# Optimization experiments

Measured on AMD Instinct MI355X. Metric: run time of the kernel, lower is better.

The kernel has to match this reference:

```python
import jax, jax.numpy as jnp
import numpy as np

S, B, T, D = 256, 32, 24, 512


def setup_inputs() -> dict:
    key = jax.random.key(0)
    ks = jax.random.split(key, 30)
    def lin(k, out_d, in_d):
        kw, kb = jax.random.split(k)
        w = jax.random.normal(kw, (out_d, in_d), jnp.float32) * 0.02
        b = jax.random.normal(kb, (out_d,), jnp.float32) * 0.02
        return w, b
    inp = {
        'context_output': jax.random.normal(ks[0], (S, B, D), jnp.float32),
        'context_hidden_state': jax.random.normal(ks[1], (B, D), jnp.float32),
        'question_output': jax.random.normal(ks[2], (T, B, D), jnp.float32),
        'question_hidden_state': jax.random.normal(ks[3], (B, D), jnp.float32),
        'image_output': jax.random.normal(ks[4], (S, B, D), jnp.float32),
        'image_hidden_state': jax.random.normal(ks[5], (B, D), jnp.float32),
    }
    inp['fc1_w'], inp['fc1_b'] = lin(ks[6], D, D)
    inp['fc2_w'], inp['fc2_b'] = lin(ks[7], D, D)
    inp['dm_w'], inp['dm_b'] = lin(ks[8], D, D)
    inp['ms_w'], inp['ms_b'] = lin(ks[9], 1, D)
    inp['rm_w'], inp['rm_b'] = lin(ks[10], D, D)
    inp['qm_w'], inp['qm_b'] = lin(ks[11], D, D)
    inp['rr_w'], inp['rr_b'] = lin(ks[12], D, D)
    inp['rg_w'], inp['rg_b'] = lin(ks[13], D, D)
    inp['qg_w'], inp['qg_b'] = lin(ks[14], D, D)
    return inp


def reference(context_output, context_hidden_state, question_output,
              question_hidden_state, image_output, image_hidden_state,
              fc1_w, fc1_b, fc2_w, fc2_b, dm_w, dm_b, ms_w, ms_b,
              rm_w, rm_b, qm_w, qm_b, rr_w, rr_b, rg_w, rg_b, qg_w, qg_b):
    # context_output/image_output: [S,B,D] -> co: [B,S,D]
    co = (jnp.einsum('sbd,ed->bse', context_output, fc1_w) + fc1_b
          + jnp.einsum('sbd,ed->bse', image_output, fc2_w) + fc2_b)
    # linear_dm(co) is loop-invariant; compute once (same math as original)
    co_dm = jnp.einsum('bsd,ed->bse', co, dm_w) + dm_b  # [B,S,D]

    def step(r, q):
        # r: [B,D] (the original's [B,1,D] memory), q: [B,D]
        add = (r @ rm_w.T + rm_b) + (q @ qm_w.T + qm_b)  # [B,D]
        m = jnp.tanh(co_dm + add[:, None, :])             # [B,S,D]
        logits = m @ ms_w.T + ms_b                        # [B,S,1]
        s = jax.nn.softmax(logits, axis=1)                # softmax over S
        r_new = jnp.sum(s * co, axis=1) + jnp.tanh(r @ rr_w.T + rr_b)
        return r_new, None

    r0 = jnp.zeros((B, D), co.dtype)
    r, _ = jax.lax.scan(step, r0, question_output)  # scan over T steps
    g = (r @ rg_w.T + rg_b) + (question_hidden_state @ qg_w.T + qg_b)
    return g
```

## Files before the change

### kernel.cpp

```cpp
#include <hip/hip_runtime.h>

#define S_DIM 256
#define B_DIM 32
#define T_DIM 24
#define D_DIM 512

typedef short short8 __attribute__((ext_vector_type(8)));
typedef unsigned short ushort8 __attribute__((ext_vector_type(8)));
typedef unsigned short ushort4v __attribute__((ext_vector_type(4)));
typedef float float4v __attribute__((ext_vector_type(4)));
typedef unsigned long long u64;

#define ATOM_ST64(p, v) __hip_atomic_store((p), (v), __ATOMIC_RELAXED, __HIP_MEMORY_SCOPE_AGENT)
#define ATOM_LD64(p)    __hip_atomic_load((p), __ATOMIC_RELAXED, __HIP_MEMORY_SCOPE_AGENT)

__device__ __forceinline__ float bf2f(unsigned short u) {
  union { unsigned int i; float f; } v; v.i = ((unsigned int)u) << 16; return v.f;
}
__device__ __forceinline__ unsigned short f2bf(float f) {
  union { float f; unsigned int i; } v; v.f = f;
  unsigned int i = v.i;
  return (unsigned short)((i + 0x7fffu + ((i >> 16) & 1u)) >> 16);
}
__device__ __forceinline__ float tanh_fast(float x) {
  float p = __builtin_amdgcn_exp2f(x * 2.885390082f);
  return 1.f - 2.f * __builtin_amdgcn_rcpf(1.f + p);
}
__device__ __forceinline__ void gload_lds16(const void* g, void* l) {
  __builtin_amdgcn_global_load_lds(
      (const __attribute__((address_space(1))) void*)g,
      (__attribute__((address_space(3))) void*)l, 16, 0, 0);
}
__device__ __forceinline__ u64 pack_tag(unsigned tag, float v) {
  union { float f; unsigned u; } c; c.f = v;
  return ((u64)tag << 32) | (u64)c.u;
}
__device__ __forceinline__ float unpack_val(u64 v) {
  union { unsigned u; float f; } c; c.u = (unsigned)v; return c.f;
}
__device__ __forceinline__ float poll_val(const u64* p, unsigned tag) {
  u64 v = ATOM_LD64(p);
  while ((unsigned)(v >> 32) != tag) { __builtin_amdgcn_s_sleep(1); v = ATOM_LD64(p); }
  return unpack_val(v);
}

__global__ __launch_bounds__(256)
void cvt_kernel(const float* __restrict__ s0, const float* __restrict__ s1,
                const float* __restrict__ s2, const float* __restrict__ s3,
                const float* __restrict__ s4,
                unsigned short* __restrict__ d0, unsigned short* __restrict__ d1,
                unsigned short* __restrict__ d2, unsigned short* __restrict__ d3,
                unsigned short* __restrict__ d4)
{
  const int idx = blockIdx.x * 256 + threadIdx.x;
  const float* s; unsigned short* d; int off;
  if (idx < 2097152) {
    off = idx & 1048575;
    if (idx < 1048576) { s = s0; d = d0; } else { s = s1; d = d1; }
  } else {
    const int k = (idx - 2097152) >> 16;
    off = (idx - 2097152) & 65535;
    if (k == 0)      { s = s2; d = d2; }
    else if (k == 1) { s = s3; d = d3; }
    else             { s = s4; d = d4; }
  }
  const float4v v = ((const float4v*)s)[off];
  ushort4v u;
  u[0] = f2bf(v[0]); u[1] = f2bf(v[1]); u[2] = f2bf(v[2]); u[3] = f2bf(v[3]);
  ((ushort4v*)d)[off] = u;
}

template<bool DUAL, bool PERMUTE>
__global__ __launch_bounds__(256)
void gemm_nt(const unsigned short* __restrict__ A1,
             const unsigned short* __restrict__ A2,
             const unsigned short* __restrict__ W1,
             const unsigned short* __restrict__ W2,
             const float* __restrict__ bias1,
             const float* __restrict__ bias2,
             unsigned short* __restrict__ out)
{
  __shared__ unsigned short At[128 * 32] __attribute__((aligned(16)));
  __shared__ unsigned short Bt[64 * 32] __attribute__((aligned(16)));

  const int tid  = threadIdx.x;
  const int wid  = tid >> 6;
  const int lane = tid & 63;
  const int bid = blockIdx.x;
  const int bm = ((bid & 7) << 3) | ((bid >> 3) & 7);
  const int bn = bid >> 6;
  const int wm = (wid & 1) * 64, wn = (wid >> 1) * 32;

  float4v acc[4][2];
#pragma unroll
  for (int i = 0; i < 4; ++i)
#pragma unroll
    for (int jj = 0; jj < 2; ++jj) acc[i][jj] = (float4v){0.f, 0.f, 0.f, 0.f};

  const int NK = DUAL ? 32 : 16;
  for (int it = 0; it < NK; ++it) {
    const int kk = it * 32;
    const unsigned short* As = A1;
    const unsigned short* Ws = W1;
    int ks = kk;
    if (DUAL && kk >= 512) { As = A2; Ws = W2; ks = kk - 512; }

    __syncthreads();
#pragma unroll
    for (int i = 0; i < 2; ++i)
      gload_lds16(As + (size_t)(bm * 128 + wid * 32 + i * 16 + (lane >> 2)) * 512 + ks + (lane & 3) * 8,
                  &At[(wid * 32 + i * 16) * 32]);
    gload_lds16(Ws + (size_t)(bn * 64 + wid * 16 + (lane >> 2)) * 512 + ks + (lane & 3) * 8,
                &Bt[(wid * 16) * 32]);
    __syncthreads();

    short8 fa[4], fb[2];
#pragma unroll
    for (int mi = 0; mi < 4; ++mi)
      fa[mi] = *(const short8*)&At[(wm + mi * 16 + (lane & 15)) * 32 + (lane >> 4) * 8];
#pragma unroll
    for (int ni = 0; ni < 2; ++ni)
      fb[ni] = *(const short8*)&Bt[(wn + ni * 16 + (lane & 15)) * 32 + (lane >> 4) * 8];
#pragma unroll
    for (int mi = 0; mi < 4; ++mi)
#pragma unroll
      for (int ni = 0; ni < 2; ++ni)
        acc[mi][ni] = __builtin_amdgcn_mfma_f32_16x16x32_bf16(fa[mi], fb[ni], acc[mi][ni], 0, 0, 0);
  }

#pragma unroll
  for (int mi = 0; mi < 4; ++mi) {
    const int row0 = wm + mi * 16 + (lane >> 4) * 4;
#pragma unroll
    for (int ni = 0; ni < 2; ++ni) {
      const int col = bn * 64 + wn + ni * 16 + (lane & 15);
      float bsum = 0.f;
      if (bias1) bsum += bias1[col];
      if (bias2) bsum += bias2[col];
#pragma unroll
      for (int i = 0; i < 4; ++i) {
        const int m = bm * 128 + row0 + i;
        const int orow = PERMUTE ? ((m & 31) * 256 + (m >> 5)) : m;
        out[(size_t)orow * 512 + col] = f2bf(acc[mi][ni][i] + bsum);
      }
    }
  }
}

__global__ __launch_bounds__(512)
void scan_kernel(const unsigned short* __restrict__ co,
                 const unsigned short* __restrict__ codm,
                 const float* __restrict__ qo,
                 u64* __restrict__ addT,
                 u64* __restrict__ rrtT,
                 u64* __restrict__ denT,
                 u64* __restrict__ pvecT,
                 const float* __restrict__ ms_w,
                 const float* __restrict__ rm_w,
                 const float* __restrict__ rr_w,
                 const float* __restrict__ rr_b,
                 const float* __restrict__ qm_w,
                 const float* __restrict__ qm_b,
                 const float* __restrict__ rm_b,
                 const float* __restrict__ qhs,
                 const float* __restrict__ rg_w,
                 const float* __restrict__ qg_w,
                 const float* __restrict__ rg_b,
                 const float* __restrict__ qg_b,
                 float* __restrict__ outg)
{
  __shared__ unsigned short scrS[32 * 520] __attribute__((aligned(16)));
  __shared__ float rS[512];
  __shared__ float addS[512] __attribute__((aligned(16)));
  __shared__ float msS[512] __attribute__((aligned(16)));
  __shared__ float partS[512];
  __shared__ float partR[512];
  __shared__ float rrtS[512];
  __shared__ float pvS[512];
  __shared__ float wS[32];
  __shared__ float rrbS[64];
  __shared__ float qmrmS[64];
  __shared__ float denS[8];
  __shared__ float qaddS[T_DIM * 64];

  const int tid  = threadIdx.x;
  const int wid  = tid >> 6;
  const int lane = tid & 63;
  const int b = blockIdx.x >> 3;
  const int j = blockIdx.x & 7;

  ushort8 rmp[8], rrp[8], qmp[8];
  for (int pass = 0; pass < 6; ++pass) {
    const float* Wsrc = (pass < 2) ? rm_w : (pass < 4) ? rr_w : qm_w;
    const int rbase = (pass & 1) * 32;
    for (int r = wid; r < 32; r += 8) {
      const float* src = &Wsrc[(size_t)(j * 64 + rbase + r) * 512 + lane * 8];
      float4v a = *(const float4v*)src;
      float4v c = *(const float4v*)(src + 4);
      ushort8 u8;
#pragma unroll
      for (int i = 0; i < 4; ++i) { u8[i] = f2bf(a[i]); u8[i + 4] = f2bf(c[i]); }
      *(ushort8*)&scrS[r * 520 + lane * 8] = u8;
    }
    __syncthreads();
    if ((lane >> 5) == (pass & 1)) {
      const int rloc = lane & 31;
#pragma unroll
      for (int u = 0; u < 8; ++u) {
        ushort8 v = *(const ushort8*)&scrS[rloc * 520 + wid * 64 + u * 8];
        if (pass < 2) rmp[u] = v; else if (pass < 4) rrp[u] = v; else qmp[u] = v;
      }
    }
    __syncthreads();
  }

  msS[tid] = ms_w[tid];
  if (tid < 64) {
    rrbS[tid]  = rr_b[j * 64 + tid];
    qmrmS[tid] = qm_b[j * 64 + tid] + rm_b[j * 64 + tid];
  }

  float* qoS = (float*)scrS;
  for (int half = 0; half < 2; ++half) {
    __syncthreads();
#pragma unroll
    for (int i = 0; i < 3; ++i) {
      const int f4 = tid + i * 512;
      const int tl = f4 >> 7, c4 = f4 & 127;
      ((float4v*)qoS)[f4] =
          *(const float4v*)&qo[((size_t)(half * 12 + tl) * 32 + b) * 512 + c4 * 4];
    }
    __syncthreads();
    for (int tl = 0; tl < 12; ++tl) {
      float p = 0.f;
#pragma unroll
      for (int u = 0; u < 8; ++u) {
        ushort8 w8 = qmp[u];
#pragma unroll
        for (int i2 = 0; i2 < 8; ++i2)
          p = fmaf(qoS[tl * 512 + wid * 64 + u * 8 + i2], bf2f(w8[i2]), p);
      }
      float* pbuf = (tl & 1) ? partR : partS;
      pbuf[wid * 64 + lane] = p;
      __syncthreads();
      if (wid == (tl & 1)) {
        float s = 0.f;
#pragma unroll
        for (int w2 = 0; w2 < 8; ++w2) s += pbuf[w2 * 64 + lane];
        qaddS[(half * 12 + tl) * 64 + lane] = s + qmrmS[lane];
      }
    }
    __syncthreads();
  }

  const size_t gbase = ((size_t)b * 256 + j * 32) * 512;
  for (int idx = tid; idx < 2048; idx += 512)
    *(ushort8*)&scrS[idx * 8] = *(const ushort8*)&codm[gbase + (size_t)idx * 8];
  const unsigned short* cdS = scrS;

  partS[tid] = 0.f;
  partR[tid] = 0.f;

  for (int t = 0; t < T_DIM; ++t) {
    const unsigned tagA = 2u * (unsigned)t + 1u;
    const unsigned tagB = 2u * (unsigned)t + 2u;
    __syncthreads();

    if (wid == 0) {
      float s = 0.f;
#pragma unroll
      for (int w2 = 0; w2 < 8; ++w2) s += partS[w2 * 64 + lane];
      s += qaddS[t * 64 + lane];
      ATOM_ST64(&addT[b * 512 + j * 64 + lane], pack_tag(tagA, s));
    } else if (wid == 1) {
      float s = 0.f;
#pragma unroll
      for (int w2 = 0; w2 < 8; ++w2) s += partR[w2 * 64 + lane];
      ATOM_ST64(&rrtT[(size_t)(t & 1) * (B_DIM * 512) + b * 512 + j * 64 + lane],
                pack_tag(tagA, tanh_fast(s + rrbS[lane])));
    }
    addS[tid] = poll_val(&addT[b * 512 + tid], tagA);
    __syncthreads();

#pragma unroll
    for (int q = 0; q < 4; ++q) {
      const int sl = wid * 4 + q;
      ushort8 cd8 = *(const ushort8*)&cdS[sl * 512 + lane * 8];
      float4v a0 = *(const float4v*)&addS[lane * 8];
      float4v a1 = *(const float4v*)&addS[lane * 8 + 4];
      float4v m0 = *(const float4v*)&msS[lane * 8];
      float4v m1 = *(const float4v*)&msS[lane * 8 + 4];
      float acc = 0.f;
#pragma unroll
      for (int i = 0; i < 4; ++i) {
        acc = fmaf(tanh_fast(bf2f(cd8[i]) + a0[i]), m0[i], acc);
        acc = fmaf(tanh_fast(bf2f(cd8[i + 4]) + a1[i]), m1[i], acc);
      }
#pragma unroll
      for (int off = 32; off > 0; off >>= 1) acc += __shfl_xor(acc, off, 64);
      if (lane == 0) wS[sl] = __builtin_amdgcn_exp2f(acc * 1.44269504f);
    }
    __syncthreads();

    {
      float accv = 0.f;
#pragma unroll 8
      for (int sl = 0; sl < 32; ++sl)
        accv = fmaf(wS[sl], bf2f(co[gbase + (size_t)sl * 512 + tid]), accv);
      ATOM_ST64(&pvecT[((size_t)b * 8 + j) * 512 + tid], pack_tag(tagB, accv));
    }
    float dv = 0.f;
    if (wid == 0) {
      dv = (lane < 32) ? wS[lane] : 0.f;
#pragma unroll
      for (int off = 32; off > 0; off >>= 1) dv += __shfl_xor(dv, off, 64);
    }
    __syncthreads();
    if (tid == 0) ATOM_ST64(&denT[b * 8 + j], pack_tag(tagB, dv));

    u64 rv64 = ATOM_LD64(&rrtT[(size_t)(t & 1) * (B_DIM * 512) + b * 512 + tid]);
    while ((unsigned)(rv64 >> 32) != tagA) {
      __builtin_amdgcn_s_sleep(1);
      rv64 = ATOM_LD64(&rrtT[(size_t)(t & 1) * (B_DIM * 512) + b * 512 + tid]);
    }
    rrtS[tid] = unpack_val(rv64);
    if (wid == 0 && lane < 8) denS[lane] = poll_val(&denT[b * 8 + lane], tagB);
    __syncthreads();

    u64 pv[8];
#pragma unroll
    for (int jj = 0; jj < 8; ++jj)
      pv[jj] = ATOM_LD64(&pvecT[((size_t)b * 8 + jj) * 512 + tid]);
    float am = 0.f, ar = 0.f;
#pragma unroll
    for (int u = 0; u < 8; ++u) {
      ushort8 wm8 = rmp[u], wr8 = rrp[u];
#pragma unroll
      for (int i2 = 0; i2 < 8; ++i2) {
        const float rv = rrtS[wid * 64 + u * 8 + i2];
        am = fmaf(rv, bf2f(wm8[i2]), am);
        ar = fmaf(rv, bf2f(wr8[i2]), ar);
      }
    }
    float sum = 0.f;
#pragma unroll
    for (int jj = 0; jj < 8; ++jj) {
      while ((unsigned)(pv[jj] >> 32) != tagB) {
        __builtin_amdgcn_s_sleep(1);
        pv[jj] = ATOM_LD64(&pvecT[((size_t)b * 8 + jj) * 512 + tid]);
      }
      sum += unpack_val(pv[jj]);
    }
    const float den = denS[0] + denS[1] + denS[2] + denS[3] +
                      denS[4] + denS[5] + denS[6] + denS[7];
    const float pvs = sum * __builtin_amdgcn_rcpf(den);
    pvS[tid] = pvs;
    rS[tid]  = pvs + rrtS[tid];
    __syncthreads();

#pragma unroll
    for (int u = 0; u < 8; ++u) {
      ushort8 wm8 = rmp[u], wr8 = rrp[u];
#pragma unroll
      for (int i2 = 0; i2 < 8; ++i2) {
        const float pvv = pvS[wid * 64 + u * 8 + i2];
        am = fmaf(pvv, bf2f(wm8[i2]), am);
        ar = fmaf(pvv, bf2f(wr8[i2]), ar);
      }
    }
    partS[wid * 64 + lane] = am;
    partR[wid * 64 + lane] = ar;
  }

  __syncthreads();
  addS[tid] = qhs[b * 512 + tid];
  __syncthreads();
  {
    const int e = j * 64 + lane;
    const float* rgp = rg_w + (size_t)e * 512 + wid * 64;
    const float* qgp = qg_w + (size_t)e * 512 + wid * 64;
    float acc = 0.f;
#pragma unroll
    for (int u = 0; u < 8; ++u) {
      float4v g0 = *(const float4v*)&rgp[u * 8];
      float4v g1 = *(const float4v*)&rgp[u * 8 + 4];
      float4v q0 = *(const float4v*)&qgp[u * 8];
      float4v q1 = *(const float4v*)&qgp[u * 8 + 4];
#pragma unroll
      for (int i2 = 0; i2 < 4; ++i2) {
        acc = fmaf(rS[wid * 64 + u * 8 + i2],     g0[i2], acc);
        acc = fmaf(rS[wid * 64 + u * 8 + 4 + i2], g1[i2], acc);
        acc = fmaf(addS[wid * 64 + u * 8 + i2],     q0[i2], acc);
        acc = fmaf(addS[wid * 64 + u * 8 + 4 + i2], q1[i2], acc);
      }
    }
    partS[wid * 64 + lane] = acc;
  }
  __syncthreads();
  if (wid == 0) {
    float s = 0.f;
#pragma unroll
    for (int w2 = 0; w2 < 8; ++w2) s += partS[w2 * 64 + lane];
    const int e = j * 64 + lane;
    s += rg_b[e] + qg_b[e];
    outg[b * 512 + e] = s;
  }
}

extern "C" void kernel_launch(void* const* d_in, const int* in_sizes, int n_in,
                              void* d_out, int out_size, void* d_ws, size_t ws_size,
                              hipStream_t stream)
{
  (void)in_sizes; (void)n_in; (void)out_size; (void)ws_size;
  const float* ctx  = (const float*)d_in[0];
  const float* qo   = (const float*)d_in[2];
  const float* qhs  = (const float*)d_in[3];
  const float* img  = (const float*)d_in[4];
  const float* fc1w = (const float*)d_in[6];
  const float* fc1b = (const float*)d_in[7];
  const float* fc2w = (const float*)d_in[8];
  const float* fc2b = (const float*)d_in[9];
  const float* dmw  = (const float*)d_in[10];
  const float* dmb  = (const float*)d_in[11];
  const float* msw  = (const float*)d_in[12];
  const float* rmw  = (const float*)d_in[14];
  const float* rmb  = (const float*)d_in[15];
  const float* qmw  = (const float*)d_in[16];
  const float* qmb  = (const float*)d_in[17];
  const float* rrw  = (const float*)d_in[18];
  const float* rrb  = (const float*)d_in[19];
  const float* rgw  = (const float*)d_in[20];
  const float* rgb  = (const float*)d_in[21];
  const float* qgw  = (const float*)d_in[22];
  const float* qgb  = (const float*)d_in[23];

  char* ws = (char*)d_ws;
  u64* addT  = (u64*)ws;
  u64* rrtT  = addT + B_DIM * 512;
  u64* denT  = rrtT + 2 * B_DIM * 512;
  u64* pvecT = denT + B_DIM * 8;
  unsigned short* co    = (unsigned short*)(pvecT + (size_t)B_DIM * 8 * 512);
  unsigned short* codm  = co + (size_t)B_DIM * S_DIM * D_DIM;
  unsigned short* ctxb  = codm + (size_t)B_DIM * S_DIM * D_DIM;
  unsigned short* imgb  = ctxb + (size_t)S_DIM * B_DIM * D_DIM;
  unsigned short* fc1wb = imgb + (size_t)S_DIM * B_DIM * D_DIM;
  unsigned short* fc2wb = fc1wb + D_DIM * D_DIM;
  unsigned short* dmwb  = fc2wb + D_DIM * D_DIM;
  const size_t tagBytes = (size_t)(131072 + 262144 + 2048 + 1048576);

  hipMemsetAsync(ws, 0, tagBytes, stream);
  cvt_kernel<<<8960, 256, 0, stream>>>(ctx, img, fc1w, fc2w, dmw,
                                       ctxb, imgb, fc1wb, fc2wb, dmwb);
  gemm_nt<true, true><<<512, 256, 0, stream>>>(
      ctxb, imgb, fc1wb, fc2wb, fc1b, fc2b, co);
  gemm_nt<false, false><<<512, 256, 0, stream>>>(
      co, nullptr, dmwb, nullptr, dmb, nullptr, codm);
  scan_kernel<<<256, 512, 0, stream>>>(co, codm, qo, addT, rrtT, denT, pvecT,
                                       msw, rmw, rrw, rrb, qmw, qmb, rmb, qhs,
                                       rgw, qgw, rgb, qgb, (float*)d_out);
}
```

Measured before the change: 376.4 us.

## Preconvert scan weights to bf16, remap blocks, and trim per-step barriers in scan

Extends the conversion kernel to also cast the rm/rr/qm/rg/qg weight matrices to bf16, so the scan kernel loads its register-resident weights directly instead of staging and converting them through shared memory. The block-to-(b,j) mapping is swapped, each block writes its own slice of the add vector locally instead of polling it, the denominator publish is moved earlier, and one barrier per step is removed with the pvec loads issued before the rr poll. Poll sleep intervals are lengthened. The rg/qg epilogue now reads bf16 weights, adding a small precision loss and a larger conversion launch.

```diff
diff --git a/kernel.cpp b/kernel.cpp
--- a/kernel.cpp
+++ b/kernel.cpp
@@ -40,17 +40,21 @@
 }
 __device__ __forceinline__ float poll_val(const u64* p, unsigned tag) {
   u64 v = ATOM_LD64(p);
-  while ((unsigned)(v >> 32) != tag) { __builtin_amdgcn_s_sleep(1); v = ATOM_LD64(p); }
+  while ((unsigned)(v >> 32) != tag) { __builtin_amdgcn_s_sleep(2); v = ATOM_LD64(p); }
   return unpack_val(v);
 }
 
 __global__ __launch_bounds__(256)
 void cvt_kernel(const float* __restrict__ s0, const float* __restrict__ s1,
                 const float* __restrict__ s2, const float* __restrict__ s3,
-                const float* __restrict__ s4,
+                const float* __restrict__ s4, const float* __restrict__ s5,
+                const float* __restrict__ s6, const float* __restrict__ s7,
+                const float* __restrict__ s8, const float* __restrict__ s9,
                 unsigned short* __restrict__ d0, unsigned short* __restrict__ d1,
                 unsigned short* __restrict__ d2, unsigned short* __restrict__ d3,
-                unsigned short* __restrict__ d4)
+                unsigned short* __restrict__ d4, unsigned short* __restrict__ d5,
+                unsigned short* __restrict__ d6, unsigned short* __restrict__ d7,
+                unsigned short* __restrict__ d8, unsigned short* __restrict__ d9)
 {
   const int idx = blockIdx.x * 256 + threadIdx.x;
   const float* s; unsigned short* d; int off;
@@ -60,9 +64,16 @@
   } else {
     const int k = (idx - 2097152) >> 16;
     off = (idx - 2097152) & 65535;
-    if (k == 0)      { s = s2; d = d2; }
-    else if (k == 1) { s = s3; d = d3; }
-    else             { s = s4; d = d4; }
+    switch (k) {
+      case 0:  s = s2; d = d2; break;
+      case 1:  s = s3; d = d3; break;
+      case 2:  s = s4; d = d4; break;
+      case 3:  s = s5; d = d5; break;
+      case 4:  s = s6; d = d6; break;
+      case 5:  s = s7; d = d7; break;
+      case 6:  s = s8; d = d8; break;
+      default: s = s9; d = d9; break;
+    }
   }
   const float4v v = ((const float4v*)s)[off];
   ushort4v u;
@@ -156,15 +167,15 @@
                  u64* __restrict__ denT,
                  u64* __restrict__ pvecT,
                  const float* __restrict__ ms_w,
-                 const float* __restrict__ rm_w,
-                 const float* __restrict__ rr_w,
+                 const unsigned short* __restrict__ rmwb,
+                 const unsigned short* __restrict__ rrwb,
+                 const unsigned short* __restrict__ qmwb,
                  const float* __restrict__ rr_b,
-                 const float* __restrict__ qm_w,
                  const float* __restrict__ qm_b,
                  const float* __restrict__ rm_b,
                  const float* __restrict__ qhs,
-                 const float* __restrict__ rg_w,
-                 const float* __restrict__ qg_w,
+                 const unsigned short* __restrict__ rgwb,
+                 const unsigned short* __restrict__ qgwb,
                  const float* __restrict__ rg_b,
                  const float* __restrict__ qg_b,
                  float* __restrict__ outg)
@@ -186,32 +197,18 @@
   const int tid  = threadIdx.x;
   const int wid  = tid >> 6;
   const int lane = tid & 63;
-  const int b = blockIdx.x >> 3;
-  const int j = blockIdx.x & 7;
+  const int b = blockIdx.x & 31;
+  const int j = blockIdx.x >> 5;
 
   ushort8 rmp[8], rrp[8], qmp[8];
-  for (int pass = 0; pass < 6; ++pass) {
-    const float* Wsrc = (pass < 2) ? rm_w : (pass < 4) ? rr_w : qm_w;
-    const int rbase = (pass & 1) * 32;
-    for (int r = wid; r < 32; r += 8) {
-      const float* src = &Wsrc[(size_t)(j * 64 + rbase + r) * 512 + lane * 8];
-      float4v a = *(const float4v*)src;
-      float4v c = *(const float4v*)(src + 4);
-      ushort8 u8;
-#pragma unroll
-      for (int i = 0; i < 4; ++i) { u8[i] = f2bf(a[i]); u8[i + 4] = f2bf(c[i]); }
-      *(ushort8*)&scrS[r * 520 + lane * 8] = u8;
-    }
-    __syncthreads();
-    if ((lane >> 5) == (pass & 1)) {
-      const int rloc = lane & 31;
-#pragma unroll
-      for (int u = 0; u < 8; ++u) {
-        ushort8 v = *(const ushort8*)&scrS[rloc * 520 + wid * 64 + u * 8];
-        if (pass < 2) rmp[u] = v; else if (pass < 4) rrp[u] = v; else qmp[u] = v;
-      }
-    }
-    __syncthreads();
+  {
+    const size_t ebase = (size_t)(j * 64 + lane) * 512 + wid * 64;
+#pragma unroll
+    for (int u = 0; u < 8; ++u) {
+      rmp[u] = *(const ushort8*)&rmwb[ebase + u * 8];
+      rrp[u] = *(const ushort8*)&rrwb[ebase + u * 8];
+      qmp[u] = *(const ushort8*)&qmwb[ebase + u * 8];
+    }
   }
 
   msS[tid] = ms_w[tid];
@@ -272,6 +269,7 @@
       for (int w2 = 0; w2 < 8; ++w2) s += partS[w2 * 64 + lane];
       s += qaddS[t * 64 + lane];
       ATOM_ST64(&addT[b * 512 + j * 64 + lane], pack_tag(tagA, s));
+      addS[j * 64 + lane] = s;
     } else if (wid == 1) {
       float s = 0.f;
 #pragma unroll
@@ -279,7 +277,7 @@
       ATOM_ST64(&rrtT[(size_t)(t & 1) * (B_DIM * 512) + b * 512 + j * 64 + lane],
                 pack_tag(tagA, tanh_fast(s + rrbS[lane])));
     }
-    addS[tid] = poll_val(&addT[b * 512 + tid], tagA);
+    if (wid != j) addS[tid] = poll_val(&addT[b * 512 + tid], tagA);
     __syncthreads();
 
 #pragma unroll
@@ -302,6 +300,12 @@
     }
     __syncthreads();
 
+    if (wid == 0) {
+      float dv = (lane < 32) ? wS[lane] : 0.f;
+#pragma unroll
+      for (int off = 32; off > 0; off >>= 1) dv += __shfl_xor(dv, off, 64);
+      if (lane == 0) ATOM_ST64(&denT[b * 8 + j], pack_tag(tagB, dv));
+    }
     {
       float accv = 0.f;
 #pragma unroll 8
@@ -309,28 +313,19 @@
         accv = fmaf(wS[sl], bf2f(co[gbase + (size_t)sl * 512 + tid]), accv);
       ATOM_ST64(&pvecT[((size_t)b * 8 + j) * 512 + tid], pack_tag(tagB, accv));
     }
-    float dv = 0.f;
-    if (wid == 0) {
-      dv = (lane < 32) ? wS[lane] : 0.f;
-#pragma unroll
-      for (int off = 32; off > 0; off >>= 1) dv += __shfl_xor(dv, off, 64);
-    }
-    __syncthreads();
-    if (tid == 0) ATOM_ST64(&denT[b * 8 + j], pack_tag(tagB, dv));
-
+
+    u64 pv[8];
+#pragma unroll
+    for (int jj = 0; jj < 8; ++jj)
+      pv[jj] = ATOM_LD64(&pvecT[((size_t)b * 8 + jj) * 512 + tid]);
     u64 rv64 = ATOM_LD64(&rrtT[(size_t)(t & 1) * (B_DIM * 512) + b * 512 + tid]);
     while ((unsigned)(rv64 >> 32) != tagA) {
-      __builtin_amdgcn_s_sleep(1);
+      __builtin_amdgcn_s_sleep(2);
       rv64 = ATOM_LD64(&rrtT[(size_t)(t & 1) * (B_DIM * 512) + b * 512 + tid]);
     }
     rrtS[tid] = unpack_val(rv64);
     if (wid == 0 && lane < 8) denS[lane] = poll_val(&denT[b * 8 + lane], tagB);
-    __syncthreads();
-
-    u64 pv[8];
-#pragma unroll
-    for (int jj = 0; jj < 8; ++jj)
-      pv[jj] = ATOM_LD64(&pvecT[((size_t)b * 8 + jj) * 512 + tid]);
+
     float am = 0.f, ar = 0.f;
 #pragma unroll
     for (int u = 0; u < 8; ++u) {
@@ -346,17 +341,17 @@
 #pragma unroll
     for (int jj = 0; jj < 8; ++jj) {
       while ((unsigned)(pv[jj] >> 32) != tagB) {
-        __builtin_amdgcn_s_sleep(1);
+        __builtin_amdgcn_s_sleep(2);
         pv[jj] = ATOM_LD64(&pvecT[((size_t)b * 8 + jj) * 512 + tid]);
       }
       sum += unpack_val(pv[jj]);
     }
+    __syncthreads();
     const float den = denS[0] + denS[1] + denS[2] + denS[3] +
                       denS[4] + denS[5] + denS[6] + denS[7];
     const float pvs = sum * __builtin_amdgcn_rcpf(den);
     pvS[tid] = pvs;
     rS[tid]  = pvs + rrtS[tid];
-    __syncthreads();
 
 #pragma unroll
     for (int u = 0; u < 8; ++u) {
@@ -376,22 +371,16 @@
   addS[tid] = qhs[b * 512 + tid];
   __syncthreads();
   {
-    const int e = j * 64 + lane;
-    const float* rgp = rg_w + (size_t)e * 512 + wid * 64;
-    const float* qgp = qg_w + (size_t)e * 512 + wid * 64;
+    const size_t ebase = (size_t)(j * 64 + lane) * 512 + wid * 64;
     float acc = 0.f;
 #pragma unroll
     for (int u = 0; u < 8; ++u) {
-      float4v g0 = *(const float4v*)&rgp[u * 8];
-      float4v g1 = *(const float4v*)&rgp[u * 8 + 4];
-      float4v q0 = *(const float4v*)&qgp[u * 8];
-      float4v q1 = *(const float4v*)&qgp[u * 8 + 4];
-#pragma unroll
-      for (int i2 = 0; i2 < 4; ++i2) {
-        acc = fmaf(rS[wid * 64 + u * 8 + i2],     g0[i2], acc);
-        acc = fmaf(rS[wid * 64 + u * 8 + 4 + i2], g1[i2], acc);
-        acc = fmaf(addS[wid * 64 + u * 8 + i2],     q0[i2], acc);
-        acc = fmaf(addS[wid * 64 + u * 8 + 4 + i2], q1[i2], acc);
+      ushort8 g8 = *(const ushort8*)&rgwb[ebase + u * 8];
+      ushort8 q8 = *(const ushort8*)&qgwb[ebase + u * 8];
+#pragma unroll
+      for (int i2 = 0; i2 < 8; ++i2) {
+        acc = fmaf(rS[wid * 64 + u * 8 + i2],   bf2f(g8[i2]), acc);
+        acc = fmaf(addS[wid * 64 + u * 8 + i2], bf2f(q8[i2]), acc);
       }
     }
     partS[wid * 64 + lane] = acc;
@@ -446,16 +435,21 @@
   unsigned short* fc1wb = imgb + (size_t)S_DIM * B_DIM * D_DIM;
   unsigned short* fc2wb = fc1wb + D_DIM * D_DIM;
   unsigned short* dmwb  = fc2wb + D_DIM * D_DIM;
+  unsigned short* rmwb  = dmwb + D_DIM * D_DIM;
+  unsigned short* rrwb  = rmwb + D_DIM * D_DIM;
+  unsigned short* qmwb  = rrwb + D_DIM * D_DIM;
+  unsigned short* rgwb  = qmwb + D_DIM * D_DIM;
+  unsigned short* qgwb  = rgwb + D_DIM * D_DIM;
   const size_t tagBytes = (size_t)(131072 + 262144 + 2048 + 1048576);
 
   hipMemsetAsync(ws, 0, tagBytes, stream);
-  cvt_kernel<<<8960, 256, 0, stream>>>(ctx, img, fc1w, fc2w, dmw,
-                                       ctxb, imgb, fc1wb, fc2wb, dmwb);
+  cvt_kernel<<<10240, 256, 0, stream>>>(ctx, img, fc1w, fc2w, dmw, rmw, rrw, qmw, rgw, qgw,
+                                        ctxb, imgb, fc1wb, fc2wb, dmwb, rmwb, rrwb, qmwb, rgwb, qgwb);
   gemm_nt<true, true><<<512, 256, 0, stream>>>(
       ctxb, imgb, fc1wb, fc2wb, fc1b, fc2b, co);
   gemm_nt<false, false><<<512, 256, 0, stream>>>(
       co, nullptr, dmwb, nullptr, dmb, nullptr, codm);
   scan_kernel<<<256, 512, 0, stream>>>(co, codm, qo, addT, rrtT, denT, pvecT,
-                                       msw, rmw, rrw, rrb, qmw, qmb, rmb, qhs,
-                                       rgw, qgw, rgb, qgb, (float*)d_out);
-}
+                                       msw, rmwb, rrwb, qmwb, rrb, qmb, rmb, qhs,
+                                       rgwb, qgwb, rgb, qgb, (float*)d_out);
+}
```

Result: slower. 417.1 us (+10.8%).
